# Kernel tuning notes

Hardware: AMD Instinct MI355X
Metric: run time of the kernel (lower is better)

The kernel has to match this reference:

```python
import jax, jax.numpy as jnp
import numpy as np

B, C_IN, C_OUT, L = 16, 512, 512, 2048
HEADS, K, U, KS, PAD = 4, 16, 1, 3, 1
VV = C_OUT // HEADS  # 128
EPS = 1e-5


def _conv1d(x, w, pad):
    # x: [B, Cin, L], w: [Cout, Cin, KS] -> [B, Cout, L]
    return jax.lax.conv_general_dilated(
        x, w, window_strides=(1,), padding=[(pad, pad)],
        dimension_numbers=('NCH', 'OIH', 'NCH'))


def _bn_eval(y, gamma, beta, mean, var):
    # inference-mode BatchNorm1d over channel axis
    scale = gamma * jax.lax.rsqrt(var + EPS)
    shift = beta - mean * scale
    return y * scale[None, :, None] + shift[None, :, None]


def setup_inputs() -> dict:
    key = jax.random.key(0)
    ks = jax.random.split(key, 8)
    std_q = 1.0 / np.sqrt(C_IN * KS)
    x = jax.random.normal(ks[0], (B, C_IN, L), dtype=jnp.float32)
    Wq = jax.random.normal(ks[1], (K * HEADS, C_IN, KS), dtype=jnp.float32) * std_q
    Wk = jax.random.normal(ks[2], (K * U, C_IN, KS), dtype=jnp.float32) * std_q
    Wv = jax.random.normal(ks[3], (VV * U, C_IN, KS), dtype=jnp.float32) * std_q
    embedding = jax.random.normal(ks[4], (K, U), dtype=jnp.float32)
    return {
        'x': x, 'Wq': Wq,
        'q_gamma': jnp.ones((K * HEADS,), jnp.float32),
        'q_beta': jnp.zeros((K * HEADS,), jnp.float32),
        'q_mean': jnp.zeros((K * HEADS,), jnp.float32),
        'q_var': jnp.ones((K * HEADS,), jnp.float32),
        'Wk': Wk, 'Wv': Wv,
        'v_gamma': jnp.ones((VV * U,), jnp.float32),
        'v_beta': jnp.zeros((VV * U,), jnp.float32),
        'v_mean': jnp.zeros((VV * U,), jnp.float32),
        'v_var': jnp.ones((VV * U,), jnp.float32),
        'embedding': embedding,
    }


def reference(x, Wq, q_gamma, q_beta, q_mean, q_var, Wk, Wv,
              v_gamma, v_beta, v_mean, v_var, embedding):
    batch, _, n = x.shape
    # projections
    q = _bn_eval(_conv1d(x, Wq, PAD), q_gamma, q_beta, q_mean, q_var)
    q = q.reshape(batch, HEADS, K, n)                      # bhkn
    keys = _conv1d(x, Wk, PAD).reshape(batch, K, U, n)     # bkun
    sm = jax.nn.softmax(keys, axis=-1)                     # softmax over positions
    v = _bn_eval(_conv1d(x, Wv, PAD), v_gamma, v_beta, v_mean, v_var)
    v = v.reshape(batch, VV, U, n)                         # bvun
    # content lambda
    lambda_c = jnp.einsum('bkun,bvun->bkv', sm, v)
    y_c = jnp.einsum('bhkn,bkv->bhvn', q, lambda_c)
    # position lambda
    lambda_p = jnp.einsum('ku,bvun->bkvn', embedding, v)
    y_p = jnp.einsum('bhkn,bkvn->bhvn', q, lambda_p)
    out = y_c + y_p
    return out.reshape(batch, HEADS * VV, n)
```

## Files before the change

kernel.cpp:

```cpp
#include <hip/hip_runtime.h>

#define BB 16
#define CIN 512
#define LLN 2048
#define EPSV 1e-5f

typedef __attribute__((ext_vector_type(8))) short bf16x8s;
typedef __attribute__((ext_vector_type(4))) float f32x4;

__device__ __forceinline__ unsigned short f2bf(float f) {
    union { float f; unsigned int i; } c; c.f = f;
    unsigned int x = c.i;
    unsigned int lsb = (x >> 16) & 1;
    x += 0x7fff + lsb;
    return (unsigned short)(x >> 16);
}
__device__ __forceinline__ unsigned int pack2bf(float a, float b) {
    return (unsigned int)f2bf(a) | ((unsigned int)f2bf(b) << 16);
}

__device__ __forceinline__ void g2l16(const void* g, void* l) {
    typedef const __attribute__((address_space(1))) unsigned int GU;
    typedef __attribute__((address_space(3))) unsigned int LU;
    __builtin_amdgcn_global_load_lds((GU*)g, (LU*)l, 16, 0, 0);
}

#define WIMG_U16 7680

__global__ __launch_bounds__(256) void prep_weights(
    const float* __restrict__ Wq, const float* __restrict__ Wk,
    const float* __restrict__ Wv, unsigned short* __restrict__ Wpk)
{
    int blk = blockIdx.x;
    int cot = blk >> 4, chunk = blk & 15;
    int ci0 = chunk * 32;
    for (int i = threadIdx.x; i < WIMG_U16; i += 256) {
        int t = i / 2560, r = i % 2560, co = r / 40, ci = r % 40;
        float val = 0.f;
        int cop = cot * 64 + co;
        if (ci < 32) {
            int cig = ci0 + ci;
            if (cop < 64)        val = Wq[((size_t)cop * 512 + cig) * 3 + t];
            else if (cop < 80)   val = Wk[((size_t)(cop - 64) * 512 + cig) * 3 + t];
            else if (cop < 208)  val = Wv[((size_t)(cop - 80) * 512 + cig) * 3 + t];
        }
        Wpk[(size_t)blk * WIMG_U16 + i] = f2bf(val);
    }
}

__global__ __launch_bounds__(256) void prep_x(
    const float* __restrict__ x, unsigned short* __restrict__ xpk)
{
    const int nt = blockIdx.x;
    const int c  = blockIdx.y;
    const int b  = blockIdx.z;
    const int tid = threadIdx.x;
    const int n = nt * 256 + tid;
    const int rp = n + 1;
    const float* xb = x + ((size_t)b * CIN + (size_t)c * 32) * LLN + n;
    unsigned int row[16];
#pragma unroll
    for (int p = 0; p < 16; p++)
        row[p] = pack2bf(xb[(size_t)(2 * p) * LLN], xb[(size_t)(2 * p + 1) * LLN]);
    unsigned short* dst = xpk + ((size_t)(b * 16 + c) * 2050 + rp) * 32;
    const int sig = (rp >> 1) & 3;
#pragma unroll
    for (int s = 0; s < 4; s++) {
        int g = (s ^ sig) * 4;
        uint4 v = make_uint4(row[g], row[g + 1], row[g + 2], row[g + 3]);
        *(uint4*)(dst + s * 8) = v;
    }
    if (nt == 0 && tid < 4)
        *(uint4*)(xpk + ((size_t)(b * 16 + c) * 2050) * 32 + tid * 8) = make_uint4(0, 0, 0, 0);
    if (nt == 7 && tid < 4)
        *(uint4*)(xpk + ((size_t)(b * 16 + c) * 2050 + 2049) * 32 + tid * 8) = make_uint4(0, 0, 0, 0);
}

__global__ __launch_bounds__(256) void conv_mfma(
    const unsigned short* __restrict__ xpk, const unsigned short* __restrict__ Wpk,
    const float* __restrict__ qg, const float* __restrict__ qb,
    const float* __restrict__ qm, const float* __restrict__ qv,
    const float* __restrict__ vg, const float* __restrict__ vb,
    const float* __restrict__ vm, const float* __restrict__ vvar,
    float* __restrict__ qbuf, float* __restrict__ kbuf, float* __restrict__ vbuf)
{
    __shared__ __align__(16) unsigned short xT[258 * 32];
    __shared__ __align__(16) unsigned short wA[WIMG_U16];
    __shared__ float sscale[64], sshift[64];

    const int tid = threadIdx.x;
    const int wave = tid >> 6, lane = tid & 63;
    const int kq = lane >> 4, lm = lane & 15;
    const int n0 = blockIdx.x * 256;
    const int cot = blockIdx.y;
    const int b = blockIdx.z;

    if (tid < 64) {
        int cop = cot * 64 + tid;
        float sc = 1.f, sh = 0.f;
        if (cop < 64) {
            float g = qg[cop], be = qb[cop], m = qm[cop], va = qv[cop];
            sc = g * rsqrtf(va + EPSV); sh = be - m * sc;
        } else if (cop >= 80 && cop < 208) {
            int cc = cop - 80;
            float g = vg[cc], be = vb[cc], m = vm[cc], va = vvar[cc];
            sc = g * rsqrtf(va + EPSV); sh = be - m * sc;
        }
        sscale[tid] = sc; sshift[tid] = sh;
    }

    f32x4 acc[4][4];
#pragma unroll
    for (int i = 0; i < 4; i++)
#pragma unroll
        for (int j = 0; j < 4; j++) acc[i][j] = (f32x4){0.f, 0.f, 0.f, 0.f};

    for (int chunk = 0; chunk < 16; chunk++) {
        __syncthreads();
        const unsigned short* wsrc = Wpk + (size_t)(cot * 16 + chunk) * WIMG_U16;
        const unsigned short* xsrc = xpk + ((size_t)(b * 16 + chunk) * 2050 + n0) * 32;
        for (int i = tid; i < 960; i += 256)
            g2l16(wsrc + (size_t)i * 8, wA + i * 8);
        for (int i = tid; i < 1032; i += 256)
            g2l16(xsrc + (size_t)i * 8, xT + i * 8);
        asm volatile("s_waitcnt vmcnt(0)" ::: "memory");
        __syncthreads();

#pragma unroll
        for (int t = 0; t < 3; t++) {
            bf16x8s aF[4];
#pragma unroll
            for (int cf = 0; cf < 4; cf++)
                aF[cf] = *(const bf16x8s*)&wA[t * 2560 + (cf * 16 + lm) * 40 + kq * 8];
#pragma unroll
            for (int fn = 0; fn < 4; fn++) {
                int lr = wave * 64 + fn * 16 + lm + t;
                int grp = kq ^ ((lr >> 1) & 3);
                bf16x8s bF = *(const bf16x8s*)&xT[lr * 32 + grp * 8];
#pragma unroll
                for (int cf = 0; cf < 4; cf++)
                    acc[cf][fn] = __builtin_amdgcn_mfma_f32_16x16x32_bf16(
                        aF[cf], bF, acc[cf][fn], 0, 0, 0);
            }
        }
    }

#pragma unroll
    for (int cf = 0; cf < 4; cf++) {
#pragma unroll
        for (int fn = 0; fn < 4; fn++) {
#pragma unroll
            for (int r = 0; r < 4; r++) {
                int col = cf * 16 + kq * 4 + r;
                int cop = cot * 64 + col;
                if (cop >= 208) continue;
                float val = acc[cf][fn][r] * sscale[col] + sshift[col];
                int nout = n0 + wave * 64 + fn * 16 + lm;
                if (cop < 64)
                    qbuf[((size_t)b * 64 + cop) * LLN + nout] = val;
                else if (cop < 80)
                    kbuf[((size_t)b * 16 + (cop - 64)) * LLN + nout] = val;
                else
                    vbuf[((size_t)b * 128 + (cop - 80)) * LLN + nout] = val;
            }
        }
    }
}

__global__ __launch_bounds__(256) void softmax_kernel(float* __restrict__ kbuf)
{
    const int row = blockIdx.x;
    float* p = kbuf + (size_t)row * LLN;
    const int tid = threadIdx.x;
    __shared__ float red[256];

    float vals[8];
    float vmax = -1e30f;
#pragma unroll
    for (int j = 0; j < 8; j++) {
        vals[j] = p[tid + j * 256];
        vmax = fmaxf(vmax, vals[j]);
    }
    red[tid] = vmax;
    __syncthreads();
    for (int s = 128; s > 0; s >>= 1) {
        if (tid < s) red[tid] = fmaxf(red[tid], red[tid + s]);
        __syncthreads();
    }
    float m = red[0];
    __syncthreads();
    float sum = 0.f;
#pragma unroll
    for (int j = 0; j < 8; j++) {
        vals[j] = __expf(vals[j] - m);
        sum += vals[j];
    }
    red[tid] = sum;
    __syncthreads();
    for (int s = 128; s > 0; s >>= 1) {
        if (tid < s) red[tid] += red[tid + s];
        __syncthreads();
    }
    float inv = 1.f / red[0];
#pragma unroll
    for (int j = 0; j < 8; j++) p[tid + j * 256] = vals[j] * inv;
}

__global__ __launch_bounds__(256) void lambdac_kernel(
    const float* __restrict__ sm, const float* __restrict__ vbuf,
    float* __restrict__ lc)
{
    const int wave = threadIdx.x >> 6;
    const int lane = threadIdx.x & 63;
    const int b = blockIdx.x >> 4;
    const int vg = blockIdx.x & 15;
    const float* ps = sm + ((size_t)b * 16 + wave * 4) * LLN;
    const float* pv = vbuf + ((size_t)b * 128 + vg * 8) * LLN;
    float acc[4][8];
#pragma unroll
    for (int k = 0; k < 4; k++)
#pragma unroll
        for (int v = 0; v < 8; v++) acc[k][v] = 0.f;
#pragma unroll
    for (int j = 0; j < 8; j++) {
        int n = (j * 64 + lane) * 4;
        float4 s4[4], v4[8];
#pragma unroll
        for (int k = 0; k < 4; k++) s4[k] = *(const float4*)&ps[(size_t)k * LLN + n];
#pragma unroll
        for (int v = 0; v < 8; v++) v4[v] = *(const float4*)&pv[(size_t)v * LLN + n];
#pragma unroll
        for (int k = 0; k < 4; k++)
#pragma unroll
            for (int v = 0; v < 8; v++)
                acc[k][v] += s4[k].x * v4[v].x + s4[k].y * v4[v].y
                           + s4[k].z * v4[v].z + s4[k].w * v4[v].w;
    }
#pragma unroll
    for (int k = 0; k < 4; k++)
#pragma unroll
        for (int v = 0; v < 8; v++) {
#pragma unroll
            for (int off = 32; off > 0; off >>= 1)
                acc[k][v] += __shfl_xor(acc[k][v], off, 64);
        }
    if (lane == 0) {
#pragma unroll
        for (int k = 0; k < 4; k++)
#pragma unroll
            for (int v = 0; v < 8; v++)
                lc[((size_t)b * 16 + wave * 4 + k) * 128 + vg * 8 + v] = acc[k][v];
    }
}

#define FT_N 256
__global__ __launch_bounds__(256) void final_kernel(
    const float* __restrict__ qbuf, const float* __restrict__ vbuf,
    const float* __restrict__ lc, const float* __restrict__ emb,
    float* __restrict__ out)
{
    __shared__ float qs[16][FT_N];
    __shared__ float lcs[16][128];
    __shared__ float es[16];
    const int tid = threadIdx.x;
    const int n0 = blockIdx.x * FT_N;
    const int h = blockIdx.y;
    const int b = blockIdx.z;

    for (int i = tid; i < 16 * FT_N; i += 256) {
        int r = i >> 8, c = i & 255;
        qs[r][c] = qbuf[((size_t)b * 64 + h * 16 + r) * LLN + n0 + c];
    }
    for (int i = tid; i < 16 * 128; i += 256)
        lcs[i >> 7][i & 127] = lc[(size_t)b * 2048 + i];
    if (tid < 16) es[tid] = emb[tid];
    __syncthreads();

    const int n = n0 + tid;
    float q[16];
    float s = 0.f;
#pragma unroll
    for (int k2 = 0; k2 < 16; k2++) {
        q[k2] = qs[k2][tid];
        s += q[k2] * es[k2];
    }
    const float* pv = vbuf + (size_t)b * 128 * LLN + n;
    float* po = out + ((size_t)b * 512 + h * 128) * LLN + n;
    for (int v = 0; v < 128; v++) {
        float lam = 0.f;
#pragma unroll
        for (int k2 = 0; k2 < 16; k2++) lam += q[k2] * lcs[k2][v];
        float vvv = pv[(size_t)v * LLN];
        po[(size_t)v * LLN] = lam + s * vvv;
    }
}

extern "C" void kernel_launch(void* const* d_in, const int* in_sizes, int n_in,
                              void* d_out, int out_size, void* d_ws, size_t ws_size,
                              hipStream_t stream)
{
    const float* x   = (const float*)d_in[0];
    const float* Wq  = (const float*)d_in[1];
    const float* qg  = (const float*)d_in[2];
    const float* qb  = (const float*)d_in[3];
    const float* qm  = (const float*)d_in[4];
    const float* qv  = (const float*)d_in[5];
    const float* Wk  = (const float*)d_in[6];
    const float* Wv  = (const float*)d_in[7];
    const float* vg  = (const float*)d_in[8];
    const float* vb  = (const float*)d_in[9];
    const float* vm  = (const float*)d_in[10];
    const float* vva = (const float*)d_in[11];
    const float* emb = (const float*)d_in[12];
    float* out = (float*)d_out;

    float* qbuf = (float*)d_ws;
    float* kbuf = qbuf + (size_t)BB * 64 * LLN;
    float* vbuf = kbuf + (size_t)BB * 16 * LLN;
    float* lcb  = vbuf + (size_t)BB * 128 * LLN;
    unsigned short* Wpk = (unsigned short*)(lcb + (size_t)BB * 16 * 128);
    unsigned short* xpk = Wpk + (size_t)64 * WIMG_U16;

    hipLaunchKernelGGL(prep_weights, dim3(64), dim3(256), 0, stream, Wq, Wk, Wv, Wpk);

    hipLaunchKernelGGL(prep_x, dim3(8, 16, 16), dim3(256), 0, stream, x, xpk);

    hipLaunchKernelGGL(conv_mfma, dim3(8, 4, 16), dim3(256), 0, stream,
                       xpk, Wpk, qg, qb, qm, qv, vg, vb, vm, vva,
                       qbuf, kbuf, vbuf);

    hipLaunchKernelGGL(softmax_kernel, dim3(BB * 16), dim3(256), 0, stream, kbuf);

    hipLaunchKernelGGL(lambdac_kernel, dim3(256), dim3(256), 0, stream,
                       kbuf, vbuf, lcb);

    hipLaunchKernelGGL(final_kernel, dim3(LLN / FT_N, 4, BB), dim3(256), 0, stream,
                       qbuf, vbuf, lcb, emb, out);
}
```

Measured before the change: 213.8 us.

## Merge prep kernels, double-buffer conv loads, fuse softmax into lambda, retile final

```diff
diff --git a/kernel.cpp b/kernel.cpp
--- a/kernel.cpp
+++ b/kernel.cpp
@@ -25,55 +25,55 @@
     __builtin_amdgcn_global_load_lds((GU*)g, (LU*)l, 16, 0, 0);
 }
 
-#define WIMG_U16 7680
-
-__global__ __launch_bounds__(256) void prep_weights(
+#define WIMG_U16 6144
+
+__global__ __launch_bounds__(256) void prep_all(
+    const float* __restrict__ x,
     const float* __restrict__ Wq, const float* __restrict__ Wk,
-    const float* __restrict__ Wv, unsigned short* __restrict__ Wpk)
-{
-    int blk = blockIdx.x;
-    int cot = blk >> 4, chunk = blk & 15;
-    int ci0 = chunk * 32;
-    for (int i = threadIdx.x; i < WIMG_U16; i += 256) {
-        int t = i / 2560, r = i % 2560, co = r / 40, ci = r % 40;
-        float val = 0.f;
-        int cop = cot * 64 + co;
-        if (ci < 32) {
-            int cig = ci0 + ci;
+    const float* __restrict__ Wv,
+    unsigned short* __restrict__ xpk, unsigned short* __restrict__ Wpk)
+{
+    const int tid = threadIdx.x;
+    if (blockIdx.z < 16) {
+        const int nt = blockIdx.x;
+        const int c  = blockIdx.y;
+        const int b  = blockIdx.z;
+        const int n = nt * 256 + tid;
+        const int rp = n + 1;
+        const float* xb = x + ((size_t)b * CIN + (size_t)c * 32) * LLN + n;
+        unsigned int row[16];
+#pragma unroll
+        for (int p = 0; p < 16; p++)
+            row[p] = pack2bf(xb[(size_t)(2 * p) * LLN], xb[(size_t)(2 * p + 1) * LLN]);
+        unsigned short* dst = xpk + ((size_t)(b * 16 + c) * 2050 + rp) * 32;
+        const int sig = (rp >> 1) & 3;
+#pragma unroll
+        for (int s = 0; s < 4; s++) {
+            int g = (s ^ sig) * 4;
+            *(uint4*)(dst + s * 8) = make_uint4(row[g], row[g + 1], row[g + 2], row[g + 3]);
+        }
+        if (nt == 0 && tid < 4)
+            *(uint4*)(xpk + ((size_t)(b * 16 + c) * 2050) * 32 + tid * 8) = make_uint4(0, 0, 0, 0);
+        if (nt == 7 && tid < 4)
+            *(uint4*)(xpk + ((size_t)(b * 16 + c) * 2050 + 2049) * 32 + tid * 8) = make_uint4(0, 0, 0, 0);
+    } else {
+        const int wblk = blockIdx.y * 8 + blockIdx.x;
+        const int img = wblk >> 1, half = wblk & 1;
+        const int cot = img >> 4, chunk = img & 15;
+        const int ci0 = chunk * 32;
+        for (int i = half * 3072 + tid; i < half * 3072 + 3072; i += 256) {
+            int t = i >> 11, r = i & 2047;
+            int cf = r >> 9, lane = (r >> 3) & 63, e = i & 7;
+            int lm = lane & 15, kq = lane >> 4;
+            int cop = cot * 64 + cf * 16 + lm;
+            int cig = ci0 + kq * 8 + e;
+            float val = 0.f;
             if (cop < 64)        val = Wq[((size_t)cop * 512 + cig) * 3 + t];
             else if (cop < 80)   val = Wk[((size_t)(cop - 64) * 512 + cig) * 3 + t];
             else if (cop < 208)  val = Wv[((size_t)(cop - 80) * 512 + cig) * 3 + t];
-        }
-        Wpk[(size_t)blk * WIMG_U16 + i] = f2bf(val);
-    }
-}
-
-__global__ __launch_bounds__(256) void prep_x(
-    const float* __restrict__ x, unsigned short* __restrict__ xpk)
-{
-    const int nt = blockIdx.x;
-    const int c  = blockIdx.y;
-    const int b  = blockIdx.z;
-    const int tid = threadIdx.x;
-    const int n = nt * 256 + tid;
-    const int rp = n + 1;
-    const float* xb = x + ((size_t)b * CIN + (size_t)c * 32) * LLN + n;
-    unsigned int row[16];
-#pragma unroll
-    for (int p = 0; p < 16; p++)
-        row[p] = pack2bf(xb[(size_t)(2 * p) * LLN], xb[(size_t)(2 * p + 1) * LLN]);
-    unsigned short* dst = xpk + ((size_t)(b * 16 + c) * 2050 + rp) * 32;
-    const int sig = (rp >> 1) & 3;
-#pragma unroll
-    for (int s = 0; s < 4; s++) {
-        int g = (s ^ sig) * 4;
-        uint4 v = make_uint4(row[g], row[g + 1], row[g + 2], row[g + 3]);
-        *(uint4*)(dst + s * 8) = v;
-    }
-    if (nt == 0 && tid < 4)
-        *(uint4*)(xpk + ((size_t)(b * 16 + c) * 2050) * 32 + tid * 8) = make_uint4(0, 0, 0, 0);
-    if (nt == 7 && tid < 4)
-        *(uint4*)(xpk + ((size_t)(b * 16 + c) * 2050 + 2049) * 32 + tid * 8) = make_uint4(0, 0, 0, 0);
+            Wpk[(size_t)img * WIMG_U16 + i] = f2bf(val);
+        }
+    }
 }
 
 __global__ __launch_bounds__(256) void conv_mfma(
@@ -84,8 +84,8 @@
     const float* __restrict__ vm, const float* __restrict__ vvar,
     float* __restrict__ qbuf, float* __restrict__ kbuf, float* __restrict__ vbuf)
 {
-    __shared__ __align__(16) unsigned short xT[258 * 32];
-    __shared__ __align__(16) unsigned short wA[WIMG_U16];
+    __shared__ __align__(16) unsigned short xT[2][258 * 32];
+    __shared__ __align__(16) unsigned short wA[2][WIMG_U16];
     __shared__ float sscale[64], sshift[64];
 
     const int tid = threadIdx.x;
@@ -94,6 +94,19 @@
     const int n0 = blockIdx.x * 256;
     const int cot = blockIdx.y;
     const int b = blockIdx.z;
+
+    const unsigned short* xpanel = xpk + ((size_t)b * 16 * 2050 + n0) * 32;
+    const unsigned short* wbase  = Wpk + (size_t)cot * 16 * WIMG_U16;
+
+#define STAGE(buf, chunk)                                                      \
+    {                                                                          \
+        const unsigned short* wsrc = wbase + (size_t)(chunk) * WIMG_U16;       \
+        const unsigned short* xsrc = xpanel + (size_t)(chunk) * 2050 * 32;     \
+        for (int i = tid; i < 768; i += 256)  g2l16(wsrc + i * 8, &wA[buf][i * 8]); \
+        for (int i = tid; i < 1032; i += 256) g2l16(xsrc + i * 8, &xT[buf][i * 8]); \
+    }
+
+    STAGE(0, 0)
 
     if (tid < 64) {
         int cop = cot * 64 + tid;
@@ -115,35 +128,34 @@
 #pragma unroll
         for (int j = 0; j < 4; j++) acc[i][j] = (f32x4){0.f, 0.f, 0.f, 0.f};
 
+    asm volatile("s_waitcnt vmcnt(0)" ::: "memory");
+    __syncthreads();
+
     for (int chunk = 0; chunk < 16; chunk++) {
-        __syncthreads();
-        const unsigned short* wsrc = Wpk + (size_t)(cot * 16 + chunk) * WIMG_U16;
-        const unsigned short* xsrc = xpk + ((size_t)(b * 16 + chunk) * 2050 + n0) * 32;
-        for (int i = tid; i < 960; i += 256)
-            g2l16(wsrc + (size_t)i * 8, wA + i * 8);
-        for (int i = tid; i < 1032; i += 256)
-            g2l16(xsrc + (size_t)i * 8, xT + i * 8);
-        asm volatile("s_waitcnt vmcnt(0)" ::: "memory");
-        __syncthreads();
+        const int cur = chunk & 1;
+        if (chunk < 15) STAGE(cur ^ 1, chunk + 1)
 
 #pragma unroll
         for (int t = 0; t < 3; t++) {
             bf16x8s aF[4];
 #pragma unroll
             for (int cf = 0; cf < 4; cf++)
-                aF[cf] = *(const bf16x8s*)&wA[t * 2560 + (cf * 16 + lm) * 40 + kq * 8];
+                aF[cf] = *(const bf16x8s*)&wA[cur][((t * 4 + cf) * 64 + lane) * 8];
 #pragma unroll
             for (int fn = 0; fn < 4; fn++) {
                 int lr = wave * 64 + fn * 16 + lm + t;
                 int grp = kq ^ ((lr >> 1) & 3);
-                bf16x8s bF = *(const bf16x8s*)&xT[lr * 32 + grp * 8];
+                bf16x8s bF = *(const bf16x8s*)&xT[cur][lr * 32 + grp * 8];
 #pragma unroll
                 for (int cf = 0; cf < 4; cf++)
                     acc[cf][fn] = __builtin_amdgcn_mfma_f32_16x16x32_bf16(
                         aF[cf], bF, acc[cf][fn], 0, 0, 0);
             }
         }
-    }
+        asm volatile("s_waitcnt vmcnt(0)" ::: "memory");
+        __syncthreads();
+    }
+#undef STAGE
 
 #pragma unroll
     for (int cf = 0; cf < 4; cf++) {
@@ -167,129 +179,127 @@
     }
 }
 
-__global__ __launch_bounds__(256) void softmax_kernel(float* __restrict__ kbuf)
-{
-    const int row = blockIdx.x;
-    float* p = kbuf + (size_t)row * LLN;
-    const int tid = threadIdx.x;
-    __shared__ float red[256];
-
-    float vals[8];
-    float vmax = -1e30f;
-#pragma unroll
-    for (int j = 0; j < 8; j++) {
-        vals[j] = p[tid + j * 256];
-        vmax = fmaxf(vmax, vals[j]);
-    }
-    red[tid] = vmax;
-    __syncthreads();
-    for (int s = 128; s > 0; s >>= 1) {
-        if (tid < s) red[tid] = fmaxf(red[tid], red[tid + s]);
-        __syncthreads();
-    }
-    float m = red[0];
-    __syncthreads();
-    float sum = 0.f;
-#pragma unroll
-    for (int j = 0; j < 8; j++) {
-        vals[j] = __expf(vals[j] - m);
-        sum += vals[j];
-    }
-    red[tid] = sum;
-    __syncthreads();
-    for (int s = 128; s > 0; s >>= 1) {
-        if (tid < s) red[tid] += red[tid + s];
-        __syncthreads();
-    }
-    float inv = 1.f / red[0];
-#pragma unroll
-    for (int j = 0; j < 8; j++) p[tid + j * 256] = vals[j] * inv;
-}
-
 __global__ __launch_bounds__(256) void lambdac_kernel(
-    const float* __restrict__ sm, const float* __restrict__ vbuf,
-    float* __restrict__ lc)
+    const float* __restrict__ kb, const float* __restrict__ vbuf,
+    float* __restrict__ lcb)
 {
     const int wave = threadIdx.x >> 6;
     const int lane = threadIdx.x & 63;
-    const int b = blockIdx.x >> 4;
-    const int vg = blockIdx.x & 15;
-    const float* ps = sm + ((size_t)b * 16 + wave * 4) * LLN;
-    const float* pv = vbuf + ((size_t)b * 128 + vg * 8) * LLN;
-    float acc[4][8];
-#pragma unroll
-    for (int k = 0; k < 4; k++)
-#pragma unroll
-        for (int v = 0; v < 8; v++) acc[k][v] = 0.f;
+    const int b = blockIdx.x >> 5;
+    const int vg = blockIdx.x & 31;
+    const float* ps = kb + ((size_t)b * 16 + wave * 4) * LLN;
+    const float* pv = vbuf + ((size_t)b * 128 + vg * 4) * LLN;
+
+    float m[4] = {-1e30f, -1e30f, -1e30f, -1e30f};
 #pragma unroll
     for (int j = 0; j < 8; j++) {
         int n = (j * 64 + lane) * 4;
-        float4 s4[4], v4[8];
-#pragma unroll
-        for (int k = 0; k < 4; k++) s4[k] = *(const float4*)&ps[(size_t)k * LLN + n];
-#pragma unroll
-        for (int v = 0; v < 8; v++) v4[v] = *(const float4*)&pv[(size_t)v * LLN + n];
-#pragma unroll
-        for (int k = 0; k < 4; k++)
-#pragma unroll
-            for (int v = 0; v < 8; v++)
-                acc[k][v] += s4[k].x * v4[v].x + s4[k].y * v4[v].y
-                           + s4[k].z * v4[v].z + s4[k].w * v4[v].w;
+#pragma unroll
+        for (int k = 0; k < 4; k++) {
+            float4 s4 = *(const float4*)&ps[(size_t)k * LLN + n];
+            m[k] = fmaxf(m[k], fmaxf(fmaxf(s4.x, s4.y), fmaxf(s4.z, s4.w)));
+        }
     }
 #pragma unroll
     for (int k = 0; k < 4; k++)
 #pragma unroll
-        for (int v = 0; v < 8; v++) {
+        for (int off = 32; off > 0; off >>= 1)
+            m[k] = fmaxf(m[k], __shfl_xor(m[k], off, 64));
+
+    float sum[4] = {0.f, 0.f, 0.f, 0.f};
+    float acc[4][4];
+#pragma unroll
+    for (int k = 0; k < 4; k++)
+#pragma unroll
+        for (int v = 0; v < 4; v++) acc[k][v] = 0.f;
+#pragma unroll
+    for (int j = 0; j < 8; j++) {
+        int n = (j * 64 + lane) * 4;
+        float4 e4[4];
+#pragma unroll
+        for (int k = 0; k < 4; k++) {
+            float4 s4 = *(const float4*)&ps[(size_t)k * LLN + n];
+            e4[k].x = __expf(s4.x - m[k]);
+            e4[k].y = __expf(s4.y - m[k]);
+            e4[k].z = __expf(s4.z - m[k]);
+            e4[k].w = __expf(s4.w - m[k]);
+            sum[k] += e4[k].x + e4[k].y + e4[k].z + e4[k].w;
+        }
+#pragma unroll
+        for (int v = 0; v < 4; v++) {
+            float4 v4 = *(const float4*)&pv[(size_t)v * LLN + n];
+#pragma unroll
+            for (int k = 0; k < 4; k++)
+                acc[k][v] += e4[k].x * v4.x + e4[k].y * v4.y
+                           + e4[k].z * v4.z + e4[k].w * v4.w;
+        }
+    }
+#pragma unroll
+    for (int k = 0; k < 4; k++) {
+#pragma unroll
+        for (int off = 32; off > 0; off >>= 1)
+            sum[k] += __shfl_xor(sum[k], off, 64);
+#pragma unroll
+        for (int v = 0; v < 4; v++)
 #pragma unroll
             for (int off = 32; off > 0; off >>= 1)
                 acc[k][v] += __shfl_xor(acc[k][v], off, 64);
-        }
+    }
     if (lane == 0) {
 #pragma unroll
-        for (int k = 0; k < 4; k++)
-#pragma unroll
-            for (int v = 0; v < 8; v++)
-                lc[((size_t)b * 16 + wave * 4 + k) * 128 + vg * 8 + v] = acc[k][v];
-    }
-}
-
-#define FT_N 256
+        for (int k = 0; k < 4; k++) {
+            float inv = 1.f / sum[k];
+#pragma unroll
+            for (int v = 0; v < 4; v++)
+                lcb[((size_t)b * 16 + wave * 4 + k) * 128 + vg * 4 + v] = acc[k][v] * inv;
+        }
+    }
+}
+
 __global__ __launch_bounds__(256) void final_kernel(
     const float* __restrict__ qbuf, const float* __restrict__ vbuf,
-    const float* __restrict__ lc, const float* __restrict__ emb,
+    const float* __restrict__ lcb, const float* __restrict__ emb,
     float* __restrict__ out)
 {
-    __shared__ float qs[16][FT_N];
-    __shared__ float lcs[16][128];
+    __shared__ float lcsT[128][16];
     __shared__ float es[16];
     const int tid = threadIdx.x;
-    const int n0 = blockIdx.x * FT_N;
-    const int h = blockIdx.y;
-    const int b = blockIdx.z;
-
-    for (int i = tid; i < 16 * FT_N; i += 256) {
-        int r = i >> 8, c = i & 255;
-        qs[r][c] = qbuf[((size_t)b * 64 + h * 16 + r) * LLN + n0 + c];
-    }
-    for (int i = tid; i < 16 * 128; i += 256)
-        lcs[i >> 7][i & 127] = lc[(size_t)b * 2048 + i];
+    const int h = tid >> 6, nl = tid & 63;
+    const int n0 = blockIdx.x * 64;
+    const int b = blockIdx.y;
+
+    for (int i = tid; i < 2048; i += 256)
+        lcsT[i >> 4][i & 15] = lcb[(size_t)b * 2048 + (size_t)(i & 15) * 128 + (i >> 4)];
     if (tid < 16) es[tid] = emb[tid];
     __syncthreads();
 
-    const int n = n0 + tid;
-    float q[16];
+    const int n = n0 + nl;
+    const float* pq = qbuf + ((size_t)b * 64 + h * 16) * LLN + n;
+    float4 q4[4];
+#pragma unroll
+    for (int kk = 0; kk < 4; kk++) {
+        q4[kk].x = pq[(size_t)(kk * 4 + 0) * LLN];
+        q4[kk].y = pq[(size_t)(kk * 4 + 1) * LLN];
+        q4[kk].z = pq[(size_t)(kk * 4 + 2) * LLN];
+        q4[kk].w = pq[(size_t)(kk * 4 + 3) * LLN];
+    }
     float s = 0.f;
 #pragma unroll
-    for (int k2 = 0; k2 < 16; k2++) {
-        q[k2] = qs[k2][tid];
-        s += q[k2] * es[k2];
-    }
+    for (int kk = 0; kk < 4; kk++)
+        s += q4[kk].x * es[kk * 4] + q4[kk].y * es[kk * 4 + 1]
+           + q4[kk].z * es[kk * 4 + 2] + q4[kk].w * es[kk * 4 + 3];
+
     const float* pv = vbuf + (size_t)b * 128 * LLN + n;
     float* po = out + ((size_t)b * 512 + h * 128) * LLN + n;
     for (int v = 0; v < 128; v++) {
-        float lam = 0.f;
-#pragma unroll
-        for (int k2 = 0; k2 < 16; k2++) lam += q[k2] * lcs[k2][v];
+        float4 c0 = *(const float4*)&lcsT[v][0];
+        float4 c1 = *(const float4*)&lcsT[v][4];
+        float4 c2 = *(const float4*)&lcsT[v][8];
+        float4 c3 = *(const float4*)&lcsT[v][12];
+        float lam = q4[0].x * c0.x + q4[0].y * c0.y + q4[0].z * c0.z + q4[0].w * c0.w
+                  + q4[1].x * c1.x + q4[1].y * c1.y + q4[1].z * c1.z + q4[1].w * c1.w
+                  + q4[2].x * c2.x + q4[2].y * c2.y + q4[2].z * c2.z + q4[2].w * c2.w
+                  + q4[3].x * c3.x + q4[3].y * c3.y + q4[3].z * c3.z + q4[3].w * c3.w;
         float vvv = pv[(size_t)v * LLN];
         po[(size_t)v * LLN] = lam + s * vvv;
     }
@@ -321,19 +331,16 @@
     unsigned short* Wpk = (unsigned short*)(lcb + (size_t)BB * 16 * 128);
     unsigned short* xpk = Wpk + (size_t)64 * WIMG_U16;
 
-    hipLaunchKernelGGL(prep_weights, dim3(64), dim3(256), 0, stream, Wq, Wk, Wv, Wpk);
-
-    hipLaunchKernelGGL(prep_x, dim3(8, 16, 16), dim3(256), 0, stream, x, xpk);
+    hipLaunchKernelGGL(prep_all, dim3(8, 16, 17), dim3(256), 0, stream,
+                       x, Wq, Wk, Wv, xpk, Wpk);
 
     hipLaunchKernelGGL(conv_mfma, dim3(8, 4, 16), dim3(256), 0, stream,
                        xpk, Wpk, qg, qb, qm, qv, vg, vb, vm, vva,
                        qbuf, kbuf, vbuf);
 
-    hipLaunchKernelGGL(softmax_kernel, dim3(BB * 16), dim3(256), 0, stream, kbuf);
-
-    hipLaunchKernelGGL(lambdac_kernel, dim3(256), dim3(256), 0, stream,
+    hipLaunchKernelGGL(lambdac_kernel, dim3(512), dim3(256), 0, stream,
                        kbuf, vbuf, lcb);
 
-    hipLaunchKernelGGL(final_kernel, dim3(LLN / FT_N, 4, BB), dim3(256), 0, stream,
+    hipLaunchKernelGGL(final_kernel, dim3(32, BB), dim3(256), 0, stream,
                        qbuf, vbuf, lcb, emb, out);
 }
```

After: 204.2 us. -4.5%, faster.
